# Optimization experiments

Measured on AMD Instinct MI355X. Metric: run time of the kernel, lower is better.

The kernel has to match this reference:

```python
import jax, jax.numpy as jnp
import numpy as np

B, E, N, M = 512, 1024, 1024, 128
EPS = 1e-16


def setup_inputs() -> dict:
    key = jax.random.key(0)
    k1, k2, k3, k4 = jax.random.split(key, 4)
    embeddings = jax.random.normal(k1, (B, E), dtype=jnp.float32)
    w_prev = jax.random.uniform(k2, (B, N), dtype=jnp.float32)
    w_prev = w_prev / jnp.sum(w_prev, axis=1, keepdims=True)  # valid attention over N slots
    memory = jax.random.normal(k3, (B, N, M), dtype=jnp.float32)
    W = jax.random.normal(k4, (E, M + 6), dtype=jnp.float32) * (1.4 / np.sqrt(0.5 * (E + M + 6)))
    b = jnp.zeros((M + 6,), dtype=jnp.float32)
    return {"embeddings": embeddings, "w_prev": w_prev, "memory": memory, "W": W, "b": b}


def reference(embeddings, w_prev, memory, W, b):
    # Dense projection to (k | beta | g | s | y), widths (M, 1, 1, 3, 1)
    params = embeddings @ W + b  # [B, M+6]
    k = params[:, :M]                       # content key [B, M]
    beta = jax.nn.softplus(params[:, M:M + 1])   # key strength >= 0
    g = jax.nn.sigmoid(params[:, M + 1:M + 2])   # interpolation gate in (0,1)
    s = jax.nn.softmax(params[:, M + 2:M + 5], axis=1)  # shift weights [B, 3]
    y = 1.0 + jax.nn.softplus(params[:, M + 5:M + 6])   # sharpening >= 1

    # Content addressing: cosine similarity of key vs each memory row
    dot = jnp.einsum('bm,bnm->bn', k, memory)  # [B, N]
    k_norm = jnp.linalg.norm(k, axis=1, keepdims=True)          # [B, 1]
    m_norm = jnp.linalg.norm(memory, axis=2)                    # [B, N]
    cos = dot / (k_norm * m_norm + EPS)
    w_c = jax.nn.softmax(beta * cos, axis=1)  # [B, N]

    # Interpolate with previous weighting
    w_g = g * w_c + (1.0 - g) * w_prev

    # Circular convolution with 3-tap shift kernel (shifts -1, 0, +1)
    w_tilde = (s[:, 0:1] * jnp.roll(w_g, 1, axis=1)
               + s[:, 1:2] * w_g
               + s[:, 2:3] * jnp.roll(w_g, -1, axis=1))

    # Sharpen
    w_pow = jnp.power(w_tilde + EPS, y)
    w = w_pow / jnp.sum(w_pow, axis=1, keepdims=True)  # memory_locations [B, N]

    # Memory read: weighted sum of rows
    memory_data = jnp.einsum('bn,bnm->bm', w, memory)  # [B, M]
    return (memory_data, w)
```

## Files before the change

kernel.cpp:

```cpp
#include <hip/hip_runtime.h>
#include <hip/hip_bf16.h>

#define B_ 512
#define E_ 1024
#define N_ 1024
#define M_ 128
#define P_ 134

__device__ __forceinline__ float softplus_f(float x) {
    return fmaxf(x, 0.f) + log1pf(expf(-fabsf(x)));
}

__global__ __launch_bounds__(256) void k_params(
    const float* __restrict__ emb, const float* __restrict__ W,
    const float* __restrict__ bias,
    float* __restrict__ k_all, float* __restrict__ knorm,
    float* __restrict__ scal)
{
    __shared__ float se[E_];
    __shared__ float sp[P_];
    __shared__ float red[2];
    const int b = blockIdx.x, t = threadIdx.x;
    for (int i = t; i < E_; i += 256) se[i] = emb[b * E_ + i];
    __syncthreads();
    if (t < P_) {
        float a0 = 0.f, a1 = 0.f, a2 = 0.f, a3 = 0.f;
        #pragma unroll 4
        for (int e = 0; e < E_; e += 4) {
            a0 = fmaf(se[e + 0], W[(e + 0) * P_ + t], a0);
            a1 = fmaf(se[e + 1], W[(e + 1) * P_ + t], a1);
            a2 = fmaf(se[e + 2], W[(e + 2) * P_ + t], a2);
            a3 = fmaf(se[e + 3], W[(e + 3) * P_ + t], a3);
        }
        sp[t] = bias[t] + ((a0 + a1) + (a2 + a3));
    }
    __syncthreads();
    if (t < 64) {
        float v = sp[t] * sp[t] + sp[t + 64] * sp[t + 64];
        #pragma unroll
        for (int m = 1; m < 64; m <<= 1) v += __shfl_xor(v, m);
        if (t == 0) red[0] = v;
    }
    __syncthreads();
    if (t < M_) k_all[b * M_ + t] = sp[t];
    if (t == 0) {
        knorm[b] = sqrtf(red[0]);
        float beta = softplus_f(sp[M_ + 0]);
        float g    = 1.f / (1.f + expf(-sp[M_ + 1]));
        float a0 = sp[M_ + 2], a1 = sp[M_ + 3], a2 = sp[M_ + 4];
        float mx = fmaxf(a0, fmaxf(a1, a2));
        float e0 = expf(a0 - mx), e1 = expf(a1 - mx), e2 = expf(a2 - mx);
        float inv = 1.f / (e0 + e1 + e2);
        float y = 1.f + softplus_f(sp[M_ + 5]);
        float* sc = &scal[b * 8];
        sc[0] = beta; sc[1] = g; sc[2] = e0 * inv; sc[3] = e1 * inv;
        sc[4] = e2 * inv; sc[5] = y;
    }
}

__global__ __launch_bounds__(256) void k_cos(
    const float* __restrict__ mem, const float* __restrict__ k_all,
    const float* __restrict__ knorm, const float* __restrict__ scal,
    float* __restrict__ z)
{
    const int wid  = blockIdx.x * 4 + (threadIdx.x >> 6);
    const int lane = threadIdx.x & 63;
    const int b    = wid >> 5;
    const int n0   = (wid & 31) * 32;
    const int half = lane >> 5, q = lane & 31;
    const float4 k4   = *(const float4*)&k_all[b * M_ + q * 4];
    const float  kn   = knorm[b];
    const float  beta = scal[b * 8];
    const float* base = mem + ((size_t)b * N_ + n0 + half) * M_ + q * 4;
    float* zb = z + b * N_ + n0 + half;
    #pragma unroll 4
    for (int i = 0; i < 16; ++i) {
        const float4 v = *(const float4*)(base + (size_t)i * 2 * M_);
        float dot = v.x * k4.x + v.y * k4.y + v.z * k4.z + v.w * k4.w;
        float sq  = v.x * v.x + v.y * v.y + v.z * v.z + v.w * v.w;
        #pragma unroll
        for (int m = 1; m < 32; m <<= 1) {
            dot += __shfl_xor(dot, m);
            sq  += __shfl_xor(sq,  m);
        }
        if (q == 0) {
            float mn = sqrtf(sq);
            zb[i * 2] = beta * dot / (kn * mn + 1e-16f);
        }
    }
}

__device__ __forceinline__ float block_sum(float v, volatile float* red, int t) {
    #pragma unroll
    for (int m = 1; m < 64; m <<= 1) v += __shfl_xor(v, m);
    __syncthreads();
    if ((t & 63) == 0) red[t >> 6] = v;
    __syncthreads();
    return red[0] + red[1] + red[2] + red[3];
}
__device__ __forceinline__ float block_max(float v, volatile float* red, int t) {
    #pragma unroll
    for (int m = 1; m < 64; m <<= 1) v = fmaxf(v, __shfl_xor(v, m));
    __syncthreads();
    if ((t & 63) == 0) red[t >> 6] = v;
    __syncthreads();
    return fmaxf(fmaxf(red[0], red[1]), fmaxf(red[2], red[3]));
}

__global__ __launch_bounds__(256) void k_weights(
    const float* __restrict__ z_in, const float* __restrict__ w_prev,
    const float* __restrict__ scal, float* __restrict__ w_out)
{
    __shared__ float wg[N_];
    __shared__ float red[4];
    const int b = blockIdx.x, t = threadIdx.x;
    const float g  = scal[b * 8 + 1];
    const float s0 = scal[b * 8 + 2], s1 = scal[b * 8 + 3], s2 = scal[b * 8 + 4];
    const float y  = scal[b * 8 + 5];
    float zv[4];
    float mx = -INFINITY;
    #pragma unroll
    for (int j = 0; j < 4; ++j) {
        zv[j] = z_in[b * N_ + t * 4 + j];
        mx = fmaxf(mx, zv[j]);
    }
    mx = block_max(mx, red, t);
    float lsum = 0.f, ev[4];
    #pragma unroll
    for (int j = 0; j < 4; ++j) { ev[j] = expf(zv[j] - mx); lsum += ev[j]; }
    float inv = 1.f / block_sum(lsum, red, t);
    #pragma unroll
    for (int j = 0; j < 4; ++j) {
        float wc = ev[j] * inv;
        wg[t * 4 + j] = g * wc + (1.f - g) * w_prev[b * N_ + t * 4 + j];
    }
    __syncthreads();
    float wp[4], psum = 0.f;
    #pragma unroll
    for (int j = 0; j < 4; ++j) {
        int n = t * 4 + j;
        float wt = s0 * wg[(n - 1) & (N_ - 1)] + s1 * wg[n] + s2 * wg[(n + 1) & (N_ - 1)];
        wp[j] = powf(wt + 1e-16f, y);
        psum += wp[j];
    }
    float pinv = 1.f / block_sum(psum, red, t);
    #pragma unroll
    for (int j = 0; j < 4; ++j) w_out[b * N_ + t * 4 + j] = wp[j] * pinv;
}

__global__ __launch_bounds__(1024) void k_read(
    const float* __restrict__ mem, const float* __restrict__ w,
    float* __restrict__ out)
{
    __shared__ float4 lds[32][32];
    const int b = blockIdx.x;
    const int t = threadIdx.x;
    const int r = t >> 5, q = t & 31;
    float4 acc = make_float4(0.f, 0.f, 0.f, 0.f);
    const float* base = mem + ((size_t)b * N_ + r) * M_ + q * 4;
    const float* wb = w + b * N_ + r;
    #pragma unroll 4
    for (int i = 0; i < 32; ++i) {
        float wv = wb[i * 32];
        const float4 v = *(const float4*)(base + (size_t)i * 32 * M_);
        acc.x = fmaf(wv, v.x, acc.x);
        acc.y = fmaf(wv, v.y, acc.y);
        acc.z = fmaf(wv, v.z, acc.z);
        acc.w = fmaf(wv, v.w, acc.w);
    }
    lds[r][q] = acc;
    __syncthreads();
    #pragma unroll
    for (int s = 16; s > 0; s >>= 1) {
        if (r < s) {
            float4 u = lds[r + s][q];
            float4 m = lds[r][q];
            m.x += u.x; m.y += u.y; m.z += u.z; m.w += u.w;
            lds[r][q] = m;
        }
        __syncthreads();
    }
    if (r == 0) {
        float4 s0 = lds[0][q];
        *(float4*)&out[b * M_ + q * 4] = s0;
    }
}

extern "C" void kernel_launch(void* const* d_in, const int* in_sizes, int n_in,
                              void* d_out, int out_size, void* d_ws, size_t ws_size,
                              hipStream_t stream) {
    const float* emb    = (const float*)d_in[0];
    const float* w_prev = (const float*)d_in[1];
    const float* mem    = (const float*)d_in[2];
    const float* W      = (const float*)d_in[3];
    const float* bias   = (const float*)d_in[4];

    float* out_md = (float*)d_out;
    float* out_w  = (float*)d_out + B_ * M_;

    float* ws    = (float*)d_ws;
    float* k_all = ws;
    float* knorm = ws + 65536;
    float* scal  = ws + 66048;

    k_params <<<B_, 256, 0, stream>>>(emb, W, bias, k_all, knorm, scal);
    k_cos    <<<4096, 256, 0, stream>>>(mem, k_all, knorm, scal, out_w);
    k_weights<<<B_, 256, 0, stream>>>(out_w, w_prev, scal, out_w);
    k_read   <<<B_, 1024, 0, stream>>>(mem, out_w, out_md);
}
```

Before: 448.1 us.

## Fuse cosine, weighting and read kernels into one per-batch kernel with memory reuse

```diff
diff --git a/kernel.cpp b/kernel.cpp
--- a/kernel.cpp
+++ b/kernel.cpp
@@ -6,6 +6,9 @@
 #define N_ 1024
 #define M_ 128
 #define P_ 134
+
+#define RLO 24
+#define LLO 18
 
 __device__ __forceinline__ float softplus_f(float x) {
     return fmaxf(x, 0.f) + log1pf(expf(-fabsf(x)));
@@ -58,23 +61,38 @@
     }
 }
 
-__global__ __launch_bounds__(256) void k_cos(
-    const float* __restrict__ mem, const float* __restrict__ k_all,
-    const float* __restrict__ knorm, const float* __restrict__ scal,
-    float* __restrict__ z)
+__global__ __launch_bounds__(1024) void k_fused(
+    const float* __restrict__ mem, const float* __restrict__ w_prev,
+    const float* __restrict__ k_all, const float* __restrict__ knorm,
+    const float* __restrict__ scal,
+    float* __restrict__ out_md, float* __restrict__ out_w)
 {
-    const int wid  = blockIdx.x * 4 + (threadIdx.x >> 6);
-    const int lane = threadIdx.x & 63;
-    const int b    = wid >> 5;
-    const int n0   = (wid & 31) * 32;
+    __shared__ float zbuf[N_];
+    __shared__ float wgbuf[N_];
+    __shared__ float red[16];
+    __shared__ float4 acc16[16][32];
+    __shared__ float cache[6][32][M_];
+
+    const int b    = blockIdx.x;
+    const int t    = threadIdx.x;
+    const int wid  = t >> 6;
+    const int lane = t & 63;
     const int half = lane >> 5, q = lane & 31;
+
     const float4 k4   = *(const float4*)&k_all[b * M_ + q * 4];
     const float  kn   = knorm[b];
-    const float  beta = scal[b * 8];
-    const float* base = mem + ((size_t)b * N_ + n0 + half) * M_ + q * 4;
-    float* zb = z + b * N_ + n0 + half;
-    #pragma unroll 4
-    for (int i = 0; i < 16; ++i) {
+    const float  beta = scal[b * 8 + 0];
+    const float  g    = scal[b * 8 + 1];
+    const float  s0   = scal[b * 8 + 2];
+    const float  s1   = scal[b * 8 + 3];
+    const float  s2   = scal[b * 8 + 4];
+    const float  y    = scal[b * 8 + 5];
+
+    const float* base = mem + ((size_t)b * N_ + wid * 64 + half) * M_ + q * 4;
+    float4 rc[8];
+
+    #pragma unroll 6
+    for (int i = 0; i < LLO; ++i) {
         const float4 v = *(const float4*)(base + (size_t)i * 2 * M_);
         float dot = v.x * k4.x + v.y * k4.y + v.z * k4.z + v.w * k4.w;
         float sq  = v.x * v.x + v.y * v.y + v.z * v.z + v.w * v.w;
@@ -83,106 +101,119 @@
             dot += __shfl_xor(dot, m);
             sq  += __shfl_xor(sq,  m);
         }
-        if (q == 0) {
-            float mn = sqrtf(sq);
-            zb[i * 2] = beta * dot / (kn * mn + 1e-16f);
-        }
-    }
-}
-
-__device__ __forceinline__ float block_sum(float v, volatile float* red, int t) {
+        if (q == 0)
+            zbuf[wid * 64 + 2 * i + half] = beta * dot / (kn * sqrtf(sq) + 1e-16f);
+    }
+    #pragma unroll
+    for (int i = LLO; i < RLO; ++i) {
+        const float4 v = *(const float4*)(base + (size_t)i * 2 * M_);
+        *(float4*)&cache[i - LLO][wid * 2 + half][q * 4] = v;
+        float dot = v.x * k4.x + v.y * k4.y + v.z * k4.z + v.w * k4.w;
+        float sq  = v.x * v.x + v.y * v.y + v.z * v.z + v.w * v.w;
+        #pragma unroll
+        for (int m = 1; m < 32; m <<= 1) {
+            dot += __shfl_xor(dot, m);
+            sq  += __shfl_xor(sq,  m);
+        }
+        if (q == 0)
+            zbuf[wid * 64 + 2 * i + half] = beta * dot / (kn * sqrtf(sq) + 1e-16f);
+    }
+    #pragma unroll
+    for (int ii = 0; ii < 8; ++ii) {
+        const int i = RLO + ii;
+        const float4 v = *(const float4*)(base + (size_t)i * 2 * M_);
+        rc[ii] = v;
+        float dot = v.x * k4.x + v.y * k4.y + v.z * k4.z + v.w * k4.w;
+        float sq  = v.x * v.x + v.y * v.y + v.z * v.z + v.w * v.w;
+        #pragma unroll
+        for (int m = 1; m < 32; m <<= 1) {
+            dot += __shfl_xor(dot, m);
+            sq  += __shfl_xor(sq,  m);
+        }
+        if (q == 0)
+            zbuf[wid * 64 + 2 * i + half] = beta * dot / (kn * sqrtf(sq) + 1e-16f);
+    }
+    __syncthreads();
+
+    float zv = zbuf[t];
+    float v = zv;
+    #pragma unroll
+    for (int m = 1; m < 64; m <<= 1) v = fmaxf(v, __shfl_xor(v, m));
+    if (lane == 0) red[wid] = v;
+    __syncthreads();
+    float mx = red[0];
+    #pragma unroll
+    for (int j = 1; j < 16; ++j) mx = fmaxf(mx, red[j]);
+    float ev = expf(zv - mx);
+    v = ev;
     #pragma unroll
     for (int m = 1; m < 64; m <<= 1) v += __shfl_xor(v, m);
     __syncthreads();
-    if ((t & 63) == 0) red[t >> 6] = v;
-    __syncthreads();
-    return red[0] + red[1] + red[2] + red[3];
-}
-__device__ __forceinline__ float block_max(float v, volatile float* red, int t) {
-    #pragma unroll
-    for (int m = 1; m < 64; m <<= 1) v = fmaxf(v, __shfl_xor(v, m));
-    __syncthreads();
-    if ((t & 63) == 0) red[t >> 6] = v;
-    __syncthreads();
-    return fmaxf(fmaxf(red[0], red[1]), fmaxf(red[2], red[3]));
-}
-
-__global__ __launch_bounds__(256) void k_weights(
-    const float* __restrict__ z_in, const float* __restrict__ w_prev,
-    const float* __restrict__ scal, float* __restrict__ w_out)
-{
-    __shared__ float wg[N_];
-    __shared__ float red[4];
-    const int b = blockIdx.x, t = threadIdx.x;
-    const float g  = scal[b * 8 + 1];
-    const float s0 = scal[b * 8 + 2], s1 = scal[b * 8 + 3], s2 = scal[b * 8 + 4];
-    const float y  = scal[b * 8 + 5];
-    float zv[4];
-    float mx = -INFINITY;
-    #pragma unroll
-    for (int j = 0; j < 4; ++j) {
-        zv[j] = z_in[b * N_ + t * 4 + j];
-        mx = fmaxf(mx, zv[j]);
-    }
-    mx = block_max(mx, red, t);
-    float lsum = 0.f, ev[4];
-    #pragma unroll
-    for (int j = 0; j < 4; ++j) { ev[j] = expf(zv[j] - mx); lsum += ev[j]; }
-    float inv = 1.f / block_sum(lsum, red, t);
-    #pragma unroll
-    for (int j = 0; j < 4; ++j) {
-        float wc = ev[j] * inv;
-        wg[t * 4 + j] = g * wc + (1.f - g) * w_prev[b * N_ + t * 4 + j];
-    }
-    __syncthreads();
-    float wp[4], psum = 0.f;
-    #pragma unroll
-    for (int j = 0; j < 4; ++j) {
-        int n = t * 4 + j;
-        float wt = s0 * wg[(n - 1) & (N_ - 1)] + s1 * wg[n] + s2 * wg[(n + 1) & (N_ - 1)];
-        wp[j] = powf(wt + 1e-16f, y);
-        psum += wp[j];
-    }
-    float pinv = 1.f / block_sum(psum, red, t);
-    #pragma unroll
-    for (int j = 0; j < 4; ++j) w_out[b * N_ + t * 4 + j] = wp[j] * pinv;
-}
-
-__global__ __launch_bounds__(1024) void k_read(
-    const float* __restrict__ mem, const float* __restrict__ w,
-    float* __restrict__ out)
-{
-    __shared__ float4 lds[32][32];
-    const int b = blockIdx.x;
-    const int t = threadIdx.x;
-    const int r = t >> 5, q = t & 31;
+    if (lane == 0) red[wid] = v;
+    __syncthreads();
+    float esum = 0.f;
+    #pragma unroll
+    for (int j = 0; j < 16; ++j) esum += red[j];
+    float wc = ev / esum;
+    wgbuf[t] = g * wc + (1.f - g) * w_prev[b * N_ + t];
+    __syncthreads();
+    float wt = s0 * wgbuf[(t - 1) & (N_ - 1)] + s1 * wgbuf[t] + s2 * wgbuf[(t + 1) & (N_ - 1)];
+    float wp = powf(wt + 1e-16f, y);
+    v = wp;
+    #pragma unroll
+    for (int m = 1; m < 64; m <<= 1) v += __shfl_xor(v, m);
+    __syncthreads();
+    if (lane == 0) red[wid] = v;
+    __syncthreads();
+    float psum = 0.f;
+    #pragma unroll
+    for (int j = 0; j < 16; ++j) psum += red[j];
+    float wfin = wp / psum;
+    zbuf[t] = wfin;
+    out_w[b * N_ + t] = wfin;
+    __syncthreads();
+
     float4 acc = make_float4(0.f, 0.f, 0.f, 0.f);
-    const float* base = mem + ((size_t)b * N_ + r) * M_ + q * 4;
-    const float* wb = w + b * N_ + r;
-    #pragma unroll 4
-    for (int i = 0; i < 32; ++i) {
-        float wv = wb[i * 32];
-        const float4 v = *(const float4*)(base + (size_t)i * 32 * M_);
-        acc.x = fmaf(wv, v.x, acc.x);
-        acc.y = fmaf(wv, v.y, acc.y);
-        acc.z = fmaf(wv, v.z, acc.z);
-        acc.w = fmaf(wv, v.w, acc.w);
-    }
-    lds[r][q] = acc;
-    __syncthreads();
-    #pragma unroll
-    for (int s = 16; s > 0; s >>= 1) {
-        if (r < s) {
-            float4 u = lds[r + s][q];
-            float4 m = lds[r][q];
-            m.x += u.x; m.y += u.y; m.z += u.z; m.w += u.w;
-            lds[r][q] = m;
-        }
-        __syncthreads();
-    }
-    if (r == 0) {
-        float4 s0 = lds[0][q];
-        *(float4*)&out[b * M_ + q * 4] = s0;
+    #pragma unroll
+    for (int ii = 7; ii >= 0; --ii) {
+        float wv = zbuf[wid * 64 + 2 * (RLO + ii) + half];
+        acc.x = fmaf(wv, rc[ii].x, acc.x);
+        acc.y = fmaf(wv, rc[ii].y, acc.y);
+        acc.z = fmaf(wv, rc[ii].z, acc.z);
+        acc.w = fmaf(wv, rc[ii].w, acc.w);
+    }
+    #pragma unroll
+    for (int i = RLO - 1; i >= LLO; --i) {
+        float wv = zbuf[wid * 64 + 2 * i + half];
+        const float4 mv = *(const float4*)&cache[i - LLO][wid * 2 + half][q * 4];
+        acc.x = fmaf(wv, mv.x, acc.x);
+        acc.y = fmaf(wv, mv.y, acc.y);
+        acc.z = fmaf(wv, mv.z, acc.z);
+        acc.w = fmaf(wv, mv.w, acc.w);
+    }
+    #pragma unroll 6
+    for (int i = LLO - 1; i >= 0; --i) {
+        float wv = zbuf[wid * 64 + 2 * i + half];
+        const float4 mv = *(const float4*)(base + (size_t)i * 2 * M_);
+        acc.x = fmaf(wv, mv.x, acc.x);
+        acc.y = fmaf(wv, mv.y, acc.y);
+        acc.z = fmaf(wv, mv.z, acc.z);
+        acc.w = fmaf(wv, mv.w, acc.w);
+    }
+    acc.x += __shfl_xor(acc.x, 32);
+    acc.y += __shfl_xor(acc.y, 32);
+    acc.z += __shfl_xor(acc.z, 32);
+    acc.w += __shfl_xor(acc.w, 32);
+    if (lane < 32) acc16[wid][q] = acc;
+    __syncthreads();
+    if (t < 32) {
+        float4 s = acc16[0][t];
+        #pragma unroll
+        for (int j = 1; j < 16; ++j) {
+            float4 u = acc16[j][t];
+            s.x += u.x; s.y += u.y; s.z += u.z; s.w += u.w;
+        }
+        *(float4*)&out_md[b * M_ + t * 4] = s;
     }
 }
 
@@ -203,8 +234,6 @@
     float* knorm = ws + 65536;
     float* scal  = ws + 66048;
 
-    k_params <<<B_, 256, 0, stream>>>(emb, W, bias, k_all, knorm, scal);
-    k_cos    <<<4096, 256, 0, stream>>>(mem, k_all, knorm, scal, out_w);
-    k_weights<<<B_, 256, 0, stream>>>(out_w, w_prev, scal, out_w);
-    k_read   <<<B_, 1024, 0, stream>>>(mem, out_w, out_md);
-}
+    k_params<<<B_, 256, 0, stream>>>(emb, W, bias, k_all, knorm, scal);
+    k_fused <<<B_, 1024, 0, stream>>>(mem, w_prev, k_all, knorm, scal, out_md, out_w);
+}
```

Result: faster. 427.3 us (-4.6%).
